# Kernel tuning notes

Measured on AMD Instinct MI355X. Metric: run time of the kernel, lower is better.

The kernel has to match this reference:

```python
import jax, jax.numpy as jnp
import numpy as np

N_WIRES = 12
BLOCK_CONFIGS = [(12, 3), (12, 3)]
HAM_OFFSET = 0.0
HAM_COEFF = 1.0
BATCH = 4096


def _sq(psi, w):
    # view statevector (B, 2^n) as (B, left, 2, right) isolating wire w
    B = psi.shape[0]
    n = N_WIRES
    return psi.reshape(B, 1 << w, 2, 1 << (n - 1 - w))


def _rx(psi, theta, w):
    s = _sq(psi, w)
    t = jnp.asarray(theta, jnp.float32).reshape(-1, 1, 1, 1) * 0.5
    out = jnp.cos(t) * s - 1j * jnp.sin(t) * jnp.flip(s, axis=2)
    return out.reshape(psi.shape)


def _ry(psi, theta, w):
    # [[c,-s],[s,c]]: new = cos*psi + sin*sgn*flip(psi), sgn = (-1, +1)
    s = _sq(psi, w)
    t = jnp.asarray(theta, jnp.float32).reshape(-1, 1, 1, 1) * 0.5
    sgn = jnp.array([-1.0, 1.0], jnp.float32).reshape(1, 1, 2, 1)
    out = jnp.cos(t) * s + jnp.sin(t) * sgn * jnp.flip(s, axis=2)
    return out.reshape(psi.shape)


def _rz(psi, theta, w):
    # diag(e^{-i t/2}, e^{+i t/2})
    s = _sq(psi, w)
    t = jnp.asarray(theta, jnp.float32).reshape(-1, 1, 1, 1) * 0.5
    z = jnp.array([-1.0, 1.0], jnp.float32).reshape(1, 1, 2, 1)
    out = s * jnp.exp(1j * (t * z).astype(jnp.complex64))
    return out.reshape(psi.shape)


def _cnot(psi, c, t):
    B = psi.shape[0]
    n = N_WIRES
    lo, hi = (c, t) if c < t else (t, c)
    s = psi.reshape(B, 1 << lo, 2, 1 << (hi - lo - 1), 2, 1 << (n - 1 - hi))
    ctrl_ax = 2 if c == lo else 4
    tgt_ax = 4 if c == lo else 2
    p0 = jax.lax.index_in_dim(s, 0, axis=ctrl_ax, keepdims=True)
    p1 = jnp.flip(jax.lax.index_in_dim(s, 1, axis=ctrl_ax, keepdims=True), axis=tgt_ax)
    out = jnp.concatenate([p0, p1], axis=ctrl_ax)
    return out.reshape(psi.shape)


def setup_inputs() -> dict:
    key = jax.random.key(0)
    k1, k2 = jax.random.split(key)
    total_encode = sum(ne for ne, _ in BLOCK_CONFIGS)
    total_ansatz = sum(ld for _, ld in BLOCK_CONFIGS)
    x = jax.random.normal(k1, (BATCH, total_encode), dtype=jnp.float32)
    ansatz_weights = jax.random.uniform(
        k2, (total_ansatz, 3, N_WIRES), dtype=jnp.float32,
        minval=-np.pi, maxval=np.pi)
    return {"x": x, "ansatz_weights": ansatz_weights}


def reference(x, ansatz_weights):
    B = x.shape[0]
    n = N_WIRES
    psi = jnp.zeros((B, 1 << n), jnp.complex64).at[:, 0].set(1.0)
    param_col = 0
    ansatz_block = 0
    for n_encode, linear_depth in BLOCK_CONFIGS:
        for j in range(n_encode):
            wire = j % n
            if param_col < x.shape[1]:
                psi = _rx(psi, x[:, param_col], wire)
            param_col += 1
        for _ in range(linear_depth):
            w = ansatz_weights[ansatz_block]
            for i in range(n):
                psi = _ry(psi, w[0, i], i)
                psi = _rz(psi, w[1, i], i)
                psi = _ry(psi, w[2, i], i)
            for i in range(n):
                psi = _cnot(psi, i, (i + 1) % n)
            ansatz_block += 1
    # <H> with H = offset + coeff * sum_i Z_i : diagonal = n - 2*popcount(k)
    probs = psi.real ** 2 + psi.imag ** 2
    k = jnp.arange(1 << n)
    pop = ((k[:, None] >> jnp.arange(n)[None, :]) & 1).sum(-1).astype(jnp.float32)
    diag = HAM_OFFSET + HAM_COEFF * (n - 2.0 * pop)
    expval = probs @ diag  # (B,)
    return expval[:, None]
```

## Files before the change

### kernel.cpp

```cpp
#include <hip/hip_runtime.h>
#include <math.h>

#define NTP 256
#define NT 256
#define NS 4096

typedef float f32x2 __attribute__((ext_vector_type(2)));

constexpr int ring_pi_c(int k) {
    int u = k ^ (k >> 1);
    u ^= u >> 2; u ^= u >> 4; u ^= u >> 8;
    int w0 = ((u >> 11) ^ u) & 1;
    return (u & 0x7FF) | (w0 << 11);
}
constexpr int ring_sigma_c(int k) {
    int s = (k ^ (k >> 1)) & 0x3FF;
    int b10 = ((k >> 10) ^ (k >> 11) ^ k) & 1;
    int b11 = ((k >> 11) ^ k) & 1;
    return s | (b10 << 10) | (b11 << 11);
}
constexpr int sig2(int m) { return m ^ ((m >> 4) & 0xF) ^ ((m >> 8) & 0xF); }

__device__ __forceinline__ void ygate(f32x2 cs_, f32x2& a0, f32x2& a1) {
    f32x2 n0, n1;
    asm("v_pk_mul_f32 %0, %3, %4 op_sel:[0,1] op_sel_hi:[1,1] neg_lo:[0,1] neg_hi:[0,1]\n\t"
        "v_pk_fma_f32 %0, %2, %4, %0 op_sel:[0,0,0] op_sel_hi:[1,0,1]\n\t"
        "v_pk_mul_f32 %1, %2, %4 op_sel:[0,1] op_sel_hi:[1,1]\n\t"
        "v_pk_fma_f32 %1, %3, %4, %1 op_sel:[0,0,0] op_sel_hi:[1,0,1]"
        : "=&v"(n0), "=&v"(n1)
        : "v"(a0), "v"(a1), "v"(cs_));
    a0 = n0; a1 = n1;
}

__device__ __forceinline__ void cdiag(f32x2 e, f32x2& a) {
    f32x2 m;
    asm("v_pk_mul_f32 %0, %1, %2 op_sel:[1,1] op_sel_hi:[0,1] neg_lo:[1,0]\n\t"
        "v_pk_fma_f32 %0, %1, %2, %0 op_sel:[0,0,0] op_sel_hi:[1,0,1]"
        : "=&v"(m) : "v"(a), "v"(e));
    a = m;
}

template<int P>
__device__ __forceinline__ void ygate_on_bit(f32x2 a[16], float2 cs_) {
    f32x2 v = f32x2{cs_.x, cs_.y};
    #pragma unroll
    for (int r = 0; r < 16; ++r)
        if (!(r & (1 << P)))
            ygate(v, a[r], a[r | (1 << P)]);
}

__global__ void prep1_kernel(const float* __restrict__ x,
                             const float* __restrict__ wts,
                             float2* __restrict__ ys,
                             float2* __restrict__ cdah,
                             float2* __restrict__ cs,
                             int total)
{
    int idx = blockIdx.x * blockDim.x + threadIdx.x;
    if (idx < total) {
        float th = 0.5f * x[idx];
        float s, c; sincosf(th, &s, &c);
        cs[idx] = make_float2(c, s);
    }
    if (idx < 72) {
        int ab = idx / 12, w = idx % 12;
        float a  = 0.5f * wts[(ab * 3 + 0) * 12 + w];
        float bb = 0.5f * wts[(ab * 3 + 1) * 12 + w];
        float g  = 0.5f * wts[(ab * 3 + 2) * 12 + w];
        float sa, ca, sb, cb, sg, cg;
        sincosf(a,  &sa, &ca);
        sincosf(bb, &sb, &cb);
        sincosf(g,  &sg, &cg);
        float A = cb * (ca * cg - sa * sg);
        float B = sb * (ca * cg + sa * sg);
        float C = cb * (sa * cg + ca * sg);
        float D = sb * (sa * cg - ca * sg);
        float cy = sqrtf(A * A + B * B);
        float sy = sqrtf(C * C + D * D);
        float f00 = atan2f(-B, A);
        float f10 = atan2f(D, C);
        ys[idx]   = make_float2(cy, sy);
        cdah[idx] = make_float2(0.5f * (f10 - f00), -0.5f * (f10 + f00));
    }
}

__global__ void prep2_kernel(const float2* __restrict__ cdah,
                             float2* __restrict__ tabs)
{
    int idx = blockIdx.x * blockDim.x + threadIdx.x;
    if (idx >= 7 * NS) return;
    int tl = idx >> 12, k = idx & (NS - 1);
    int sk = ring_sigma_c(k);
    const float QP = 0.7853981633974483f;
    float ph = 0.f;
    for (int w = 0; w < 12; ++w) {
        float zd = ((k  >> (11 - w)) & 1) ? 1.f : -1.f;
        float zc = ((sk >> (11 - w)) & 1) ? 1.f : -1.f;
        float dcf, ccf;
        if (tl == 3)      { dcf = QP;                       ccf = cdah[2 * 12 + w].x; }
        else if (tl == 4) { dcf = cdah[3 * 12 + w].y - QP;  ccf = 0.f; }
        else {
            int ald = (tl < 3) ? tl : tl - 1;
            dcf = cdah[ald * 12 + w].y;
            ccf = (tl == 0) ? 0.f : cdah[((tl < 3) ? tl - 1 : tl - 2) * 12 + w].x;
        }
        ph += zd * dcf + zc * ccf;
    }
    float s, c; sincosf(ph, &s, &c);
    tabs[idx] = make_float2(c, s);
}

__global__ __launch_bounds__(NT, 2)
void tqhea_kernel(const float2* __restrict__ ys,
                  const float2* __restrict__ cs,
                  const f32x2*  __restrict__ tabs,
                  float* __restrict__ out)
{
    __shared__ f32x2 psi[NS];

    const int b = blockIdx.x;
    const int t = threadIdx.x;

    const int lo = t & 0xF, h = t >> 4;
    const int tb     = (t & 0xF0) | (lo ^ h);
    const int baseP1 = (h << 8) | (lo ^ h);
    const int baseP2 = (t << 4) | (lo ^ h);
    const int Qt     = sig2(ring_pi_c(t << 4));
    const int Pt     = ring_pi_c(t << 4);

    const float2* csb  = cs + b * 24;
    const float2* cs12 = csb + 12;

    {
        float2 rc[12];
        #pragma unroll
        for (int i = 0; i < 12; ++i) rc[i] = csb[i];
        float mlo = 1.f;
        #pragma unroll
        for (int bit = 0; bit < 8; ++bit)
            mlo *= ((t >> bit) & 1) ? rc[11 - bit].y : rc[11 - bit].x;
        int pct = __popc(t);
        #pragma unroll
        for (int r = 0; r < 16; ++r) {
            float mhi = 1.f;
            #pragma unroll
            for (int p = 0; p < 4; ++p)
                mhi *= ((r >> p) & 1) ? rc[3 - p].y : rc[3 - p].x;
            float mag = mhi * mlo;
            int pc = (pct + __popc(r)) & 3;
            f32x2 v;
            v.x = (pc == 0) ? mag : ((pc == 2) ? -mag : 0.f);
            v.y = (pc == 1) ? -mag : ((pc == 3) ? mag : 0.f);
            psi[(r << 8) | (tb ^ r)] = v;
        }
    }
    __syncthreads();

    float acc = 0.f;

    #pragma unroll 1
    for (int lay = 0; lay < 7; ++lay) {
        const bool isx = (lay == 3);
        const float2* yrow = isx ? cs12 : ys + ((lay < 3) ? lay : lay - 1) * 12;
        const f32x2* Tl = tabs + lay * NS;
        f32x2 a[16];

        f32x2 e[16];
        #pragma unroll
        for (int r = 0; r < 16; ++r) e[r] = Tl[(r << 8) | t];
        #pragma unroll
        for (int r = 0; r < 16; ++r) a[r] = psi[(r << 8) | (tb ^ r)];
        #pragma unroll
        for (int r = 0; r < 16; ++r) cdiag(e[r], a[r]);
        ygate_on_bit<3>(a, yrow[0]);
        ygate_on_bit<2>(a, yrow[1]);
        ygate_on_bit<1>(a, yrow[2]);
        ygate_on_bit<0>(a, yrow[3]);
        #pragma unroll
        for (int r = 0; r < 16; ++r) psi[(r << 8) | (tb ^ r)] = a[r];
        __syncthreads();

        #pragma unroll
        for (int r = 0; r < 16; ++r) a[r] = psi[baseP1 ^ (17 * r)];
        ygate_on_bit<3>(a, yrow[4]);
        ygate_on_bit<2>(a, yrow[5]);
        ygate_on_bit<1>(a, yrow[6]);
        ygate_on_bit<0>(a, yrow[7]);
        #pragma unroll
        for (int r = 0; r < 16; ++r) psi[baseP1 ^ (17 * r)] = a[r];
        __syncthreads();

        #pragma unroll
        for (int r = 0; r < 16; ++r) a[r] = psi[baseP2 ^ r];
        if (lay < 6 && !isx) __syncthreads();
        ygate_on_bit<3>(a, yrow[8]);
        ygate_on_bit<2>(a, yrow[9]);
        ygate_on_bit<1>(a, yrow[10]);
        ygate_on_bit<0>(a, yrow[11]);
        if (lay == 6) {
            #pragma unroll
            for (int r = 0; r < 16; ++r) {
                float d = 12.0f - 2.0f * (float)__popc(Pt ^ ring_pi_c(r));
                acc += (a[r].x * a[r].x + a[r].y * a[r].y) * d;
            }
        } else if (isx) {
            #pragma unroll
            for (int r = 0; r < 16; ++r) psi[baseP2 ^ r] = a[r];
            __syncthreads();
        } else {
            #pragma unroll
            for (int r = 0; r < 16; ++r) psi[Qt ^ sig2(ring_pi_c(r))] = a[r];
            __syncthreads();
        }
    }

    #pragma unroll
    for (int off = 32; off > 0; off >>= 1)
        acc += __shfl_down(acc, off);
    __syncthreads();
    if ((t & 63) == 0) ((float*)psi)[t >> 6] = acc;
    __syncthreads();
    if (t == 0) {
        const float* rb = (const float*)psi;
        out[b] = rb[0] + rb[1] + rb[2] + rb[3];
    }
}

extern "C" void kernel_launch(void* const* d_in, const int* in_sizes, int n_in,
                              void* d_out, int out_size, void* d_ws, size_t ws_size,
                              hipStream_t stream) {
    const float* x   = (const float*)d_in[0];
    const float* wts = (const float*)d_in[1];
    float* out = (float*)d_out;
    int B = in_sizes[0] / 24;
    int total = B * 24;

    char* ws = (char*)d_ws;
    float2* ys   = (float2*)(ws);
    float2* cdah = (float2*)(ws + 576);
    float2* cs   = (float2*)(ws + 1152);
    float2* tabs = (float2*)(ws + 1152 + (size_t)total * 8);

    prep1_kernel<<<dim3((total + NTP - 1) / NTP), dim3(NTP), 0, stream>>>(x, wts, ys, cdah, cs, total);
    prep2_kernel<<<dim3((7 * NS + NTP - 1) / NTP), dim3(NTP), 0, stream>>>(cdah, tabs);
    tqhea_kernel<<<dim3(B), dim3(NT), 0, stream>>>(ys, cs, (const f32x2*)tabs, out);
}
```

Measured before the change: 202.2 us.

## Process two batch samples per block, reusing phase tables and prefetching next layer

Each block now simulates two statevectors in two shared-memory buffers. The per-layer diagonal phase table is loaded once and applied to both, and the next layer's table is prefetched during the last gate stage. Interleaving the two samples' gate work is meant to hide LDS latency and cut the table loads and barriers per sample. The costs are double the LDS per block, launch bounds lowered to 1, higher register pressure, and an assumption that B is even.

```diff
diff --git a/kernel.cpp b/kernel.cpp
--- a/kernel.cpp
+++ b/kernel.cpp
@@ -47,6 +47,13 @@
     for (int r = 0; r < 16; ++r)
         if (!(r & (1 << P)))
             ygate(v, a[r], a[r | (1 << P)]);
+}
+
+__device__ __forceinline__ void ygates4(f32x2 a[16], const float2* __restrict__ yrow, int o) {
+    ygate_on_bit<3>(a, yrow[o + 0]);
+    ygate_on_bit<2>(a, yrow[o + 1]);
+    ygate_on_bit<1>(a, yrow[o + 2]);
+    ygate_on_bit<0>(a, yrow[o + 3]);
 }
 
 __global__ void prep1_kernel(const float* __restrict__ x,
@@ -110,16 +117,41 @@
     tabs[idx] = make_float2(c, s);
 }
 
-__global__ __launch_bounds__(NT, 2)
+__device__ __forceinline__ void init_psi(f32x2* __restrict__ p, const float2* __restrict__ csb,
+                                         int t, int tb) {
+    float2 rc[12];
+    #pragma unroll
+    for (int i = 0; i < 12; ++i) rc[i] = csb[i];
+    float mlo = 1.f;
+    #pragma unroll
+    for (int bit = 0; bit < 8; ++bit)
+        mlo *= ((t >> bit) & 1) ? rc[11 - bit].y : rc[11 - bit].x;
+    int pct = __popc(t);
+    #pragma unroll
+    for (int r = 0; r < 16; ++r) {
+        float mhi = 1.f;
+        #pragma unroll
+        for (int q = 0; q < 4; ++q)
+            mhi *= ((r >> q) & 1) ? rc[3 - q].y : rc[3 - q].x;
+        float mag = mhi * mlo;
+        int pc = (pct + __popc(r)) & 3;
+        f32x2 v;
+        v.x = (pc == 0) ? mag : ((pc == 2) ? -mag : 0.f);
+        v.y = (pc == 1) ? -mag : ((pc == 3) ? mag : 0.f);
+        p[(r << 8) | (tb ^ r)] = v;
+    }
+}
+
+__global__ __launch_bounds__(NT, 1)
 void tqhea_kernel(const float2* __restrict__ ys,
                   const float2* __restrict__ cs,
                   const f32x2*  __restrict__ tabs,
                   float* __restrict__ out)
 {
-    __shared__ f32x2 psi[NS];
-
-    const int b = blockIdx.x;
-    const int t = threadIdx.x;
+    __shared__ f32x2 psi[2][NS];
+
+    const int b0 = blockIdx.x << 1;
+    const int t  = threadIdx.x;
 
     const int lo = t & 0xF, h = t >> 4;
     const int tb     = (t & 0xF0) | (lo ^ h);
@@ -128,101 +160,107 @@
     const int Qt     = sig2(ring_pi_c(t << 4));
     const int Pt     = ring_pi_c(t << 4);
 
-    const float2* csb  = cs + b * 24;
-    const float2* cs12 = csb + 12;
-
-    {
-        float2 rc[12];
-        #pragma unroll
-        for (int i = 0; i < 12; ++i) rc[i] = csb[i];
-        float mlo = 1.f;
-        #pragma unroll
-        for (int bit = 0; bit < 8; ++bit)
-            mlo *= ((t >> bit) & 1) ? rc[11 - bit].y : rc[11 - bit].x;
-        int pct = __popc(t);
-        #pragma unroll
-        for (int r = 0; r < 16; ++r) {
-            float mhi = 1.f;
-            #pragma unroll
-            for (int p = 0; p < 4; ++p)
-                mhi *= ((r >> p) & 1) ? rc[3 - p].y : rc[3 - p].x;
-            float mag = mhi * mlo;
-            int pc = (pct + __popc(r)) & 3;
-            f32x2 v;
-            v.x = (pc == 0) ? mag : ((pc == 2) ? -mag : 0.f);
-            v.y = (pc == 1) ? -mag : ((pc == 3) ? mag : 0.f);
-            psi[(r << 8) | (tb ^ r)] = v;
-        }
-    }
+    const float2* cs_0  = cs + b0 * 24;
+    const float2* cs_1  = cs_0 + 24;
+    const float2* cs12_0 = cs_0 + 12;
+    const float2* cs12_1 = cs_1 + 12;
+
+    init_psi(psi[0], cs_0, t, tb);
+    init_psi(psi[1], cs_1, t, tb);
+
+    f32x2 e[16];
+    #pragma unroll
+    for (int r = 0; r < 16; ++r) e[r] = tabs[(r << 8) | t];
     __syncthreads();
 
-    float acc = 0.f;
+    float acc0 = 0.f, acc1 = 0.f;
 
     #pragma unroll 1
     for (int lay = 0; lay < 7; ++lay) {
         const bool isx = (lay == 3);
-        const float2* yrow = isx ? cs12 : ys + ((lay < 3) ? lay : lay - 1) * 12;
-        const f32x2* Tl = tabs + lay * NS;
-        f32x2 a[16];
-
-        f32x2 e[16];
-        #pragma unroll
-        for (int r = 0; r < 16; ++r) e[r] = Tl[(r << 8) | t];
-        #pragma unroll
-        for (int r = 0; r < 16; ++r) a[r] = psi[(r << 8) | (tb ^ r)];
-        #pragma unroll
-        for (int r = 0; r < 16; ++r) cdiag(e[r], a[r]);
-        ygate_on_bit<3>(a, yrow[0]);
-        ygate_on_bit<2>(a, yrow[1]);
-        ygate_on_bit<1>(a, yrow[2]);
-        ygate_on_bit<0>(a, yrow[3]);
-        #pragma unroll
-        for (int r = 0; r < 16; ++r) psi[(r << 8) | (tb ^ r)] = a[r];
+        const float2* yrow0 = isx ? cs12_0 : ys + ((lay < 3) ? lay : lay - 1) * 12;
+        const float2* yrow1 = isx ? cs12_1 : yrow0;
+        f32x2 a0[16], a1[16];
+
+        #pragma unroll
+        for (int r = 0; r < 16; ++r) a0[r] = psi[0][(r << 8) | (tb ^ r)];
+        #pragma unroll
+        for (int r = 0; r < 16; ++r) a1[r] = psi[1][(r << 8) | (tb ^ r)];
+        #pragma unroll
+        for (int r = 0; r < 16; ++r) cdiag(e[r], a0[r]);
+        ygates4(a0, yrow0, 0);
+        #pragma unroll
+        for (int r = 0; r < 16; ++r) psi[0][(r << 8) | (tb ^ r)] = a0[r];
+        #pragma unroll
+        for (int r = 0; r < 16; ++r) cdiag(e[r], a1[r]);
+        ygates4(a1, yrow1, 0);
+        #pragma unroll
+        for (int r = 0; r < 16; ++r) psi[1][(r << 8) | (tb ^ r)] = a1[r];
         __syncthreads();
 
         #pragma unroll
-        for (int r = 0; r < 16; ++r) a[r] = psi[baseP1 ^ (17 * r)];
-        ygate_on_bit<3>(a, yrow[4]);
-        ygate_on_bit<2>(a, yrow[5]);
-        ygate_on_bit<1>(a, yrow[6]);
-        ygate_on_bit<0>(a, yrow[7]);
-        #pragma unroll
-        for (int r = 0; r < 16; ++r) psi[baseP1 ^ (17 * r)] = a[r];
+        for (int r = 0; r < 16; ++r) a0[r] = psi[0][baseP1 ^ (17 * r)];
+        #pragma unroll
+        for (int r = 0; r < 16; ++r) a1[r] = psi[1][baseP1 ^ (17 * r)];
+        ygates4(a0, yrow0, 4);
+        #pragma unroll
+        for (int r = 0; r < 16; ++r) psi[0][baseP1 ^ (17 * r)] = a0[r];
+        ygates4(a1, yrow1, 4);
+        #pragma unroll
+        for (int r = 0; r < 16; ++r) psi[1][baseP1 ^ (17 * r)] = a1[r];
         __syncthreads();
 
         #pragma unroll
-        for (int r = 0; r < 16; ++r) a[r] = psi[baseP2 ^ r];
-        if (lay < 6 && !isx) __syncthreads();
-        ygate_on_bit<3>(a, yrow[8]);
-        ygate_on_bit<2>(a, yrow[9]);
-        ygate_on_bit<1>(a, yrow[10]);
-        ygate_on_bit<0>(a, yrow[11]);
+        for (int r = 0; r < 16; ++r) a0[r] = psi[0][baseP2 ^ r];
+        #pragma unroll
+        for (int r = 0; r < 16; ++r) a1[r] = psi[1][baseP2 ^ r];
+        if (lay < 6) {
+            const f32x2* Tn = tabs + (lay + 1) * NS;
+            #pragma unroll
+            for (int r = 0; r < 16; ++r) e[r] = Tn[(r << 8) | t];
+        }
+        ygates4(a0, yrow0, 8);
         if (lay == 6) {
+            ygates4(a1, yrow1, 8);
             #pragma unroll
             for (int r = 0; r < 16; ++r) {
                 float d = 12.0f - 2.0f * (float)__popc(Pt ^ ring_pi_c(r));
-                acc += (a[r].x * a[r].x + a[r].y * a[r].y) * d;
+                acc0 += (a0[r].x * a0[r].x + a0[r].y * a0[r].y) * d;
+                acc1 += (a1[r].x * a1[r].x + a1[r].y * a1[r].y) * d;
             }
         } else if (isx) {
             #pragma unroll
-            for (int r = 0; r < 16; ++r) psi[baseP2 ^ r] = a[r];
+            for (int r = 0; r < 16; ++r) psi[0][baseP2 ^ r] = a0[r];
+            ygates4(a1, yrow1, 8);
+            #pragma unroll
+            for (int r = 0; r < 16; ++r) psi[1][baseP2 ^ r] = a1[r];
             __syncthreads();
         } else {
-            #pragma unroll
-            for (int r = 0; r < 16; ++r) psi[Qt ^ sig2(ring_pi_c(r))] = a[r];
+            __syncthreads();
+            #pragma unroll
+            for (int r = 0; r < 16; ++r) psi[0][Qt ^ sig2(ring_pi_c(r))] = a0[r];
+            ygates4(a1, yrow1, 8);
+            #pragma unroll
+            for (int r = 0; r < 16; ++r) psi[1][Qt ^ sig2(ring_pi_c(r))] = a1[r];
             __syncthreads();
         }
     }
 
     #pragma unroll
-    for (int off = 32; off > 0; off >>= 1)
-        acc += __shfl_down(acc, off);
+    for (int off = 32; off > 0; off >>= 1) {
+        acc0 += __shfl_down(acc0, off);
+        acc1 += __shfl_down(acc1, off);
+    }
     __syncthreads();
-    if ((t & 63) == 0) ((float*)psi)[t >> 6] = acc;
+    if ((t & 63) == 0) {
+        ((float*)psi)[t >> 6]     = acc0;
+        ((float*)psi)[4 + (t >> 6)] = acc1;
+    }
     __syncthreads();
     if (t == 0) {
         const float* rb = (const float*)psi;
-        out[b] = rb[0] + rb[1] + rb[2] + rb[3];
+        out[b0]     = rb[0] + rb[1] + rb[2] + rb[3];
+        out[b0 + 1] = rb[4] + rb[5] + rb[6] + rb[7];
     }
 }
 
@@ -243,5 +281,5 @@
 
     prep1_kernel<<<dim3((total + NTP - 1) / NTP), dim3(NTP), 0, stream>>>(x, wts, ys, cdah, cs, total);
     prep2_kernel<<<dim3((7 * NS + NTP - 1) / NTP), dim3(NTP), 0, stream>>>(cdah, tabs);
-    tqhea_kernel<<<dim3(B), dim3(NT), 0, stream>>>(ys, cs, (const f32x2*)tabs, out);
-}
+    tqhea_kernel<<<dim3(B / 2), dim3(NT), 0, stream>>>(ys, cs, (const f32x2*)tabs, out);
+}
```

Measured after the change: 262.8 us. +30.0%, slower.

## Use 512 threads with 8 amplitudes each and four 3-qubit passes per layer

Applied to the files above, without the earlier changes.

Doubles the block size from 256 to 512 threads, so each thread holds 8 amplitudes instead of 16 and applies gates over 3 qubits per pass, giving four passes per layer instead of three. The previous 4-bit-block XOR scheme is replaced by a new bit swizzle meant to avoid LDS bank conflicts under the new index patterns. The aim is more wave-level parallelism and lower register pressure per thread. In exchange it adds one more pass of shared-memory traffic and an extra barrier per layer, and launch bounds allow only one block per SIMD group.

```diff
diff --git a/kernel.cpp b/kernel.cpp
--- a/kernel.cpp
+++ b/kernel.cpp
@@ -2,7 +2,7 @@
 #include <math.h>
 
 #define NTP 256
-#define NT 256
+#define NT 512
 #define NS 4096
 
 typedef float f32x2 __attribute__((ext_vector_type(2)));
@@ -19,7 +19,10 @@
     int b11 = ((k >> 11) ^ k) & 1;
     return s | (b10 << 10) | (b11 << 11);
 }
-constexpr int sig2(int m) { return m ^ ((m >> 4) & 0xF) ^ ((m >> 8) & 0xF); }
+constexpr int swz(int k) {
+    int e4 = (k >> 4) & 1, e5 = (k >> 5) & 1, e6 = (k >> 6) & 1;
+    return k ^ (e4 | (e5 << 1) | (e6 << 2) | ((e4 ^ e6) << 3));
+}
 
 __device__ __forceinline__ void ygate(f32x2 cs_, f32x2& a0, f32x2& a1) {
     f32x2 n0, n1;
@@ -41,10 +44,10 @@
 }
 
 template<int P>
-__device__ __forceinline__ void ygate_on_bit(f32x2 a[16], float2 cs_) {
+__device__ __forceinline__ void ygate8(f32x2 a[8], float2 cs_) {
     f32x2 v = f32x2{cs_.x, cs_.y};
     #pragma unroll
-    for (int r = 0; r < 16; ++r)
+    for (int r = 0; r < 8; ++r)
         if (!(r & (1 << P)))
             ygate(v, a[r], a[r | (1 << P)]);
 }
@@ -110,7 +113,7 @@
     tabs[idx] = make_float2(c, s);
 }
 
-__global__ __launch_bounds__(NT, 2)
+__global__ __launch_bounds__(NT, 1)
 void tqhea_kernel(const float2* __restrict__ ys,
                   const float2* __restrict__ cs,
                   const f32x2*  __restrict__ tabs,
@@ -121,12 +124,9 @@
     const int b = blockIdx.x;
     const int t = threadIdx.x;
 
-    const int lo = t & 0xF, h = t >> 4;
-    const int tb     = (t & 0xF0) | (lo ^ h);
-    const int baseP1 = (h << 8) | (lo ^ h);
-    const int baseP2 = (t << 4) | (lo ^ h);
-    const int Qt     = sig2(ring_pi_c(t << 4));
-    const int Pt     = ring_pi_c(t << 4);
+    const int tsw = swz(t);
+    const int sQt = swz(ring_pi_c(t << 3));
+    const int Pt  = ring_pi_c(t << 3);
 
     const float2* csb  = cs + b * 24;
     const float2* cs12 = csb + 12;
@@ -135,23 +135,23 @@
         float2 rc[12];
         #pragma unroll
         for (int i = 0; i < 12; ++i) rc[i] = csb[i];
-        float mlo = 1.f;
-        #pragma unroll
-        for (int bit = 0; bit < 8; ++bit)
-            mlo *= ((t >> bit) & 1) ? rc[11 - bit].y : rc[11 - bit].x;
-        int pct = __popc(t);
-        #pragma unroll
-        for (int r = 0; r < 16; ++r) {
-            float mhi = 1.f;
-            #pragma unroll
-            for (int p = 0; p < 4; ++p)
-                mhi *= ((r >> p) & 1) ? rc[3 - p].y : rc[3 - p].x;
-            float mag = mhi * mlo;
-            int pc = (pct + __popc(r)) & 3;
+        float mlan = 1.f;
+        #pragma unroll
+        for (int bit = 0; bit < 9; ++bit)
+            mlan *= ((t >> bit) & 1) ? rc[11 - bit].y : rc[11 - bit].x;
+        int q = __popc(t);
+        #pragma unroll
+        for (int r = 0; r < 8; ++r) {
+            float mr = 1.f;
+            #pragma unroll
+            for (int p = 0; p < 3; ++p)
+                mr *= ((r >> p) & 1) ? rc[2 - p].y : rc[2 - p].x;
+            float mag = mr * mlan;
+            int pc = (q + __popc(r)) & 3;
             f32x2 v;
             v.x = (pc == 0) ? mag : ((pc == 2) ? -mag : 0.f);
             v.y = (pc == 1) ? -mag : ((pc == 3) ? mag : 0.f);
-            psi[(r << 8) | (tb ^ r)] = v;
+            psi[(r << 9) | tsw] = v;
         }
     }
     __syncthreads();
@@ -162,54 +162,67 @@
     for (int lay = 0; lay < 7; ++lay) {
         const bool isx = (lay == 3);
         const float2* yrow = isx ? cs12 : ys + ((lay < 3) ? lay : lay - 1) * 12;
-        const f32x2* Tl = tabs + lay * NS;
-        f32x2 a[16];
-
-        f32x2 e[16];
-        #pragma unroll
-        for (int r = 0; r < 16; ++r) e[r] = Tl[(r << 8) | t];
-        #pragma unroll
-        for (int r = 0; r < 16; ++r) a[r] = psi[(r << 8) | (tb ^ r)];
-        #pragma unroll
-        for (int r = 0; r < 16; ++r) cdiag(e[r], a[r]);
-        ygate_on_bit<3>(a, yrow[0]);
-        ygate_on_bit<2>(a, yrow[1]);
-        ygate_on_bit<1>(a, yrow[2]);
-        ygate_on_bit<0>(a, yrow[3]);
-        #pragma unroll
-        for (int r = 0; r < 16; ++r) psi[(r << 8) | (tb ^ r)] = a[r];
+        f32x2 a[8], e[8];
+
+        #pragma unroll
+        for (int r = 0; r < 8; ++r) e[r] = tabs[lay * NS + (r << 9) + t];
+        #pragma unroll
+        for (int r = 0; r < 8; ++r) a[r] = psi[(r << 9) | tsw];
+        #pragma unroll
+        for (int r = 0; r < 8; ++r) cdiag(e[r], a[r]);
+        ygate8<2>(a, yrow[0]);
+        ygate8<1>(a, yrow[1]);
+        ygate8<0>(a, yrow[2]);
+        #pragma unroll
+        for (int r = 0; r < 8; ++r) psi[(r << 9) | tsw] = a[r];
         __syncthreads();
 
-        #pragma unroll
-        for (int r = 0; r < 16; ++r) a[r] = psi[baseP1 ^ (17 * r)];
-        ygate_on_bit<3>(a, yrow[4]);
-        ygate_on_bit<2>(a, yrow[5]);
-        ygate_on_bit<1>(a, yrow[6]);
-        ygate_on_bit<0>(a, yrow[7]);
-        #pragma unroll
-        for (int r = 0; r < 16; ++r) psi[baseP1 ^ (17 * r)] = a[r];
+        int a1[8];
+        #pragma unroll
+        for (int r = 0; r < 8; ++r)
+            a1[r] = swz(((t >> 6) << 9) | (r << 6) | (t & 63));
+        #pragma unroll
+        for (int r = 0; r < 8; ++r) a[r] = psi[a1[r]];
+        ygate8<2>(a, yrow[3]);
+        ygate8<1>(a, yrow[4]);
+        ygate8<0>(a, yrow[5]);
+        #pragma unroll
+        for (int r = 0; r < 8; ++r) psi[a1[r]] = a[r];
         __syncthreads();
 
-        #pragma unroll
-        for (int r = 0; r < 16; ++r) a[r] = psi[baseP2 ^ r];
-        if (lay < 6 && !isx) __syncthreads();
-        ygate_on_bit<3>(a, yrow[8]);
-        ygate_on_bit<2>(a, yrow[9]);
-        ygate_on_bit<1>(a, yrow[10]);
-        ygate_on_bit<0>(a, yrow[11]);
+        int a2[8];
+        #pragma unroll
+        for (int r = 0; r < 8; ++r)
+            a2[r] = swz(((t >> 3) << 6) | (r << 3) | (t & 7));
+        #pragma unroll
+        for (int r = 0; r < 8; ++r) a[r] = psi[a2[r]];
+        ygate8<2>(a, yrow[6]);
+        ygate8<1>(a, yrow[7]);
+        ygate8<0>(a, yrow[8]);
+        #pragma unroll
+        for (int r = 0; r < 8; ++r) psi[a2[r]] = a[r];
+        __syncthreads();
+
+        const int base3 = swz(t << 3);
+        #pragma unroll
+        for (int r = 0; r < 8; ++r) a[r] = psi[base3 ^ r];
+        ygate8<2>(a, yrow[9]);
+        ygate8<1>(a, yrow[10]);
+        ygate8<0>(a, yrow[11]);
         if (lay == 6) {
             #pragma unroll
-            for (int r = 0; r < 16; ++r) {
+            for (int r = 0; r < 8; ++r) {
                 float d = 12.0f - 2.0f * (float)__popc(Pt ^ ring_pi_c(r));
                 acc += (a[r].x * a[r].x + a[r].y * a[r].y) * d;
             }
         } else if (isx) {
             #pragma unroll
-            for (int r = 0; r < 16; ++r) psi[baseP2 ^ r] = a[r];
+            for (int r = 0; r < 8; ++r) psi[base3 ^ r] = a[r];
             __syncthreads();
         } else {
-            #pragma unroll
-            for (int r = 0; r < 16; ++r) psi[Qt ^ sig2(ring_pi_c(r))] = a[r];
+            __syncthreads();
+            #pragma unroll
+            for (int r = 0; r < 8; ++r) psi[sQt ^ ring_pi_c(r)] = a[r];
             __syncthreads();
         }
     }
@@ -222,7 +235,7 @@
     __syncthreads();
     if (t == 0) {
         const float* rb = (const float*)psi;
-        out[b] = rb[0] + rb[1] + rb[2] + rb[3];
+        out[b] = rb[0] + rb[1] + rb[2] + rb[3] + rb[4] + rb[5] + rb[6] + rb[7];
     }
 }
 
```

After: 193.1 us. 4.5% less time.
